# Kernel optimization log

Hardware: AMD Instinct MI355X
Metric: run time of the kernel (lower is better)

The kernel has to match this reference:

```python
import jax, jax.numpy as jnp
import numpy as np

N_NODES = 20000   # N
N_EDGES = 320000  # E (avg degree 16)
T_STEPS = 16      # T
IN_FEATS = 1      # F
HG = 64           # hidden_g
HT = 128          # hidden_t
LN_EPS = 1e-5


def _layer_norm(x, g, b):
    mu = jnp.mean(x, axis=-1, keepdims=True)
    var = jnp.mean((x - mu) ** 2, axis=-1, keepdims=True)
    return (x - mu) * jax.lax.rsqrt(var + LN_EPS) * g + b


def setup_inputs() -> dict:
    key = jax.random.key(0)
    k = jax.random.split(key, 16)
    r = lambda i, shape, s: jax.random.normal(k[i], shape, jnp.float32) * s
    return dict(
        x_seq=jax.random.normal(k[0], (1, T_STEPS, N_NODES, IN_FEATS), jnp.float32),
        edge_index=jax.random.randint(k[1], (2, N_EDGES), 0, N_NODES, dtype=jnp.int32),
        # SAGEConv layer 0: lin_l (aggregated neighbors, has bias) + lin_r (root)
        W_l0=r(2, (IN_FEATS, HG), 0.5), W_r0=r(3, (IN_FEATS, HG), 0.5), b0=jnp.zeros((HG,), jnp.float32),
        ln0_g=jnp.ones((HG,), jnp.float32), ln0_b=jnp.zeros((HG,), jnp.float32),
        # SAGEConv layer 1
        W_l1=r(4, (HG, HG), 0.1), W_r1=r(5, (HG, HG), 0.1), b1=jnp.zeros((HG,), jnp.float32),
        ln1_g=jnp.ones((HG,), jnp.float32), ln1_b=jnp.zeros((HG,), jnp.float32),
        # GRU (torch layout: gates r,z,n stacked along first dim)
        gru_Wih=r(6, (3 * HT, HG), 0.05), gru_Whh=r(7, (3 * HT, HT), 0.05),
        gru_bih=jnp.zeros((3 * HT,), jnp.float32), gru_bhh=jnp.zeros((3 * HT,), jnp.float32),
        # head
        head_W=r(8, (HT, 1), 0.05), head_b=jnp.zeros((1,), jnp.float32),
    )


def reference(x_seq, edge_index, W_l0, W_r0, b0, ln0_g, ln0_b,
              W_l1, W_r1, b1, ln1_g, ln1_b,
              gru_Wih, gru_Whh, gru_bih, gru_bhh, head_W, head_b):
    src, dst = edge_index[0], edge_index[1]
    # in-degree for mean aggregation (clamped to 1, like PyG mean aggr on isolated nodes)
    deg = jnp.clip(jax.ops.segment_sum(jnp.ones((N_EDGES,), jnp.float32), dst,
                                       num_segments=N_NODES), 1.0)[:, None]

    def sage(x, Wl, Wr, b):
        # mean over incoming neighbors, then lin_l(aggr) + lin_r(root)
        agg = jax.ops.segment_sum(x[src], dst, num_segments=N_NODES) / deg
        return agg @ Wl + x @ Wr + b

    def stack(xt):  # xt: (N, F) -> (N, HG); dropout is identity in eval mode
        h = jax.nn.relu(_layer_norm(sage(xt, W_l0, W_r0, b0), ln0_g, ln0_b))
        h = jax.nn.relu(_layer_norm(sage(h, W_l1, W_r1, b1), ln1_g, ln1_b))
        return h

    X = x_seq[0]  # (T, N, F), B == 1
    # scan over timesteps (matches the per-t Python loop, bounds peak memory)
    _, H = jax.lax.scan(lambda c, xt: (c, stack(xt)), None, X)  # H: (T, N, HG)

    def gru_step(h, xt):  # torch GRU cell; batch = N nodes
        gi = xt @ gru_Wih.T + gru_bih
        gh = h @ gru_Whh.T + gru_bhh
        ir, iz, inn = jnp.split(gi, 3, axis=-1)
        hr, hz, hn = jnp.split(gh, 3, axis=-1)
        r = jax.nn.sigmoid(ir + hr)
        z = jax.nn.sigmoid(iz + hz)
        n = jnp.tanh(inn + r * hn)
        return (1.0 - z) * n + z * h, None

    h0 = jnp.zeros((N_NODES, HT), x_seq.dtype)
    hT, _ = jax.lax.scan(gru_step, h0, H)
    y = (hT @ head_W + head_b)[:, 0]  # (N,)
    return y
```

## Files before the change

kernel.cpp:

```cpp
#include <hip/hip_runtime.h>
#include <math.h>

#define NN 20000
#define NE 320000
#define TS 16
#define HG 64
#define HTT 128
#define NG 384
#define LN_EPS 1e-5f
#define ASTR 1032

typedef __attribute__((ext_vector_type(8))) _Float16 f16x8;
typedef __attribute__((ext_vector_type(4))) _Float16 f16x4;
typedef __attribute__((ext_vector_type(4))) float f32x4;

__device__ __forceinline__ float wave_sum64(float v) {
  #pragma unroll
  for (int off = 32; off > 0; off >>= 1) v += __shfl_xor(v, off, 64);
  return v;
}
__device__ __forceinline__ float quad_sum16(float v) {
  #pragma unroll
  for (int off = 1; off < 16; off <<= 1) v += __shfl_xor(v, off, 64);
  return v;
}
__device__ __forceinline__ float fast_sigmoid(float x) {
  return __builtin_amdgcn_rcpf(1.f + __expf(-x));
}
__device__ __forceinline__ float fast_tanh(float x) {
  float e = __expf(-2.f * fabsf(x));
  float th = (1.f - e) * __builtin_amdgcn_rcpf(1.f + e);
  return copysignf(th, x);
}

__global__ __launch_bounds__(256) void k_setup(
    const float* __restrict__ x_seq, float* __restrict__ xT,
    const float* __restrict__ Wih, _Float16* __restrict__ WihF,
    const float* __restrict__ Whh, _Float16* __restrict__ WhhF,
    const float* __restrict__ Wl1, const float* __restrict__ Wr1,
    _Float16* __restrict__ Wchi, _Float16* __restrict__ Wclo,
    const float* __restrict__ Wl0, const float* __restrict__ Wr0,
    const float* __restrict__ b0, const float* __restrict__ g0,
    const float* __restrict__ be0, float* __restrict__ P,
    int* __restrict__ cnt) {
  int gid = blockIdx.x * 256 + threadIdx.x;
  int stride = gridDim.x * 256;
  for (int i = gid; i < NN * TS; i += stride) {
    int t = i / NN, n = i - t * NN;
    xT[n * 16 + t] = x_seq[i];
  }
  for (int i = gid; i < NG * HG; i += stride) WihF[i] = (_Float16)Wih[i];
  for (int i = gid; i < NG * HTT; i += stride) WhhF[i] = (_Float16)Whh[i];
  for (int i = gid; i < HG * 128; i += stride) {
    int n = i >> 7, k = i & 127;
    float x = (k < HG) ? Wl1[k * HG + n] : Wr1[(k - HG) * HG + n];
    _Float16 h = (_Float16)x;
    Wchi[i] = h;
    Wclo[i] = (_Float16)(x - (float)h);
  }
  for (int i = gid; i < NN; i += stride) cnt[i] = 0;
  if (blockIdx.x == 0 && threadIdx.x < 64) {
    int f = threadIdx.x;
    float u = Wl0[f], v = Wr0[f], c = b0[f], g = g0[f];
    float um = wave_sum64(u) * (1.f / 64.f);
    float vm = wave_sum64(v) * (1.f / 64.f);
    float cm = wave_sum64(c) * (1.f / 64.f);
    float uc = u - um, vc = v - vm, cc = c - cm;
    float muu = wave_sum64(uc * uc) * (1.f / 64.f);
    float mvv = wave_sum64(vc * vc) * (1.f / 64.f);
    float mcc = wave_sum64(cc * cc) * (1.f / 64.f);
    float muv = wave_sum64(uc * vc) * (1.f / 64.f);
    float muc = wave_sum64(uc * cc) * (1.f / 64.f);
    float mvc = wave_sum64(vc * cc) * (1.f / 64.f);
    P[f] = uc * g; P[64 + f] = vc * g; P[128 + f] = cc * g; P[192 + f] = be0[f];
    if (f == 0) {
      P[256] = muu; P[257] = mvv; P[258] = mcc;
      P[259] = muv; P[260] = muc; P[261] = mvc;
    }
  }
}

__global__ void k_hist(const int* __restrict__ dst, int* cnt) {
  int e = blockIdx.x * blockDim.x + threadIdx.x;
  if (e < NE) atomicAdd(&cnt[dst[e]], 1);
}

__global__ void k_scan(int* cnt, int* row_ptr, float* deg_inv) {
  __shared__ int s[1024];
  const int PER = 20;
  int tid = threadIdx.x;
  int base = tid * PER;
  int vloc[PER], dloc[PER];
  int sum = 0;
  #pragma unroll
  for (int j = 0; j < PER; j++) {
    int n = base + j;
    int d = (n < NN) ? cnt[n] : 0;
    vloc[j] = sum;
    dloc[j] = d;
    sum += d;
  }
  s[tid] = sum;
  __syncthreads();
  for (int off = 1; off < 1024; off <<= 1) {
    int t = (tid >= off) ? s[tid - off] : 0;
    __syncthreads();
    s[tid] += t;
    __syncthreads();
  }
  int excl = s[tid] - sum;
  #pragma unroll
  for (int j = 0; j < PER; j++) {
    int n = base + j;
    if (n < NN) {
      int rp = excl + vloc[j];
      row_ptr[n] = rp;
      cnt[n] = rp;
      int d = dloc[j];
      deg_inv[n] = 1.0f / (float)((d > 1) ? d : 1);
    }
  }
  if (tid == 1023) row_ptr[NN] = s[1023];
}

__global__ void k_fill(const int* __restrict__ src, const int* __restrict__ dst,
                       int* cursor, int* col) {
  int e = blockIdx.x * blockDim.x + threadIdx.x;
  if (e < NE) {
    int p = atomicAdd(&cursor[dst[e]], 1);
    col[p] = src[e];
  }
}

__global__ __launch_bounds__(256) void k_h0_fused(
    const float* __restrict__ xT,
    const int* __restrict__ row_ptr, const int* __restrict__ col,
    const float* __restrict__ deg_inv,
    const float* __restrict__ P,
    _Float16* __restrict__ h0r,
    _Float16* __restrict__ code) {
  int lane = threadIdx.x & 63;
  int n = blockIdx.x * 4 + (threadIdx.x >> 6);
  int grp = lane >> 4, tl = lane & 15;
  int beg = row_ptr[n];
  int deg = row_ptr[n + 1] - beg;
  float s0 = 0.f, s1 = 0.f;
  int iters = (deg + 7) >> 3;
  for (int it = 0; it < iters; it++) {
    int e0 = it * 8 + grp, e1 = it * 8 + 4 + grp;
    bool v0 = e0 < deg, v1 = e1 < deg;
    int i0 = v0 ? e0 : 0, i1 = v1 ? e1 : 0;
    int c0 = col[beg + i0];
    int c1 = col[beg + i1];
    float x0 = xT[c0 * 16 + tl];
    float x1 = xT[c1 * 16 + tl];
    s0 += v0 ? x0 : 0.f;
    s1 += v1 ? x1 : 0.f;
  }
  float s = s0 + s1;
  s += __shfl_xor(s, 16, 64);
  s += __shfl_xor(s, 32, 64);
  float aggv = s * deg_inv[n];
  float xv = xT[n * 16 + tl];
  float muu = P[256], mvv = P[257], mcc = P[258];
  float muv = P[259], muc = P[260], mvc = P[261];
  if (lane < 16) {
    float a = aggv, x = xv;
    float var = a * a * muu + x * x * mvv + mcc
              + 2.f * (a * x * muv + a * muc + x * mvc);
    float rstd = rsqrtf(var + LN_EPS);
    f16x4 cw;
    cw[0] = (_Float16)(a * rstd);
    cw[1] = (_Float16)(x * rstd);
    cw[2] = (_Float16)rstd;
    cw[3] = (_Float16)0.f;
    *(f16x4*)&code[(size_t)n * 64 + (lane & 7) * 8 + (lane >> 3) * 4] = cw;
  }
  #pragma unroll
  for (int half = 0; half < 2; half++) {
    int c = lane + half * 64;
    int t = c >> 3, f8 = (c & 7) * 8;
    float a = __shfl(aggv, t, 64);
    float x = __shfl(xv, t, 64);
    float var = a * a * muu + x * x * mvv + mcc
              + 2.f * (a * x * muv + a * muc + x * mvc);
    float rstd = rsqrtf(var + LN_EPS);
    f16x8 o;
    #pragma unroll
    for (int j = 0; j < 8; j++) {
      int f = f8 + j;
      float d = a * P[f] + x * P[64 + f] + P[128 + f];
      o[j] = (_Float16)fmaxf(d * rstd + P[192 + f], 0.f);
    }
    *(f16x8*)&h0r[(size_t)n * 1024 + c * 8] = o;
  }
}

__global__ __launch_bounds__(256) void k_sage_fused(
    const _Float16* __restrict__ h0r,
    const int* __restrict__ row_ptr, const int* __restrict__ col,
    const _Float16* __restrict__ code,
    const float* __restrict__ P,
    const _Float16* __restrict__ Wchi, const _Float16* __restrict__ Wclo,
    const float* __restrict__ b1, const float* __restrict__ g1, const float* __restrict__ be1,
    _Float16* __restrict__ Ht_all) {
  __shared__ _Float16 aggL[16 * ASTR];
  int tid = threadIdx.x;
  int lane = tid & 63, wave = tid >> 6;
  int col16 = lane & 15, quad = lane >> 4;
  int m0 = blockIdx.x * 16;

  {
    int f1 = (lane & 7) * 8;
    float Pu[8], Pv[8], Pc[8], Pb[8];
    #pragma unroll
    for (int j = 0; j < 8; j++) {
      Pu[j] = P[f1 + j];
      Pv[j] = P[64 + f1 + j];
      Pc[j] = P[128 + f1 + j];
      Pb[j] = P[192 + f1 + j];
    }
    int codeoff = (lane >> 3) * 8;

    int i4 = lane >> 4;
    int slot = lane & 15;
    int ni = m0 + wave * 4 + i4;
    int beg_i = row_ptr[ni];
    int d_i = row_ptr[ni + 1] - beg_i;
    int cv0 = (slot < d_i) ? col[beg_i + slot] : 0;
    int cv1 = (slot + 16 < d_i) ? col[beg_i + 16 + slot] : 0;
    int dL[4], bgL[4];
    #pragma unroll
    for (int i = 0; i < 4; i++) {
      dL[i] = __builtin_amdgcn_readlane(d_i, i << 4);
      bgL[i] = __builtin_amdgcn_readlane(beg_i, i << 4);
    }

    for (int i = 0; i < 4; i++) {
      float acc1[8], acc2[8];
      #pragma unroll
      for (int j = 0; j < 8; j++) { acc1[j] = 0.f; acc2[j] = 0.f; }

      auto accum = [&](f16x8 cd) {
        float A1 = (float)cd[0], X1 = (float)cd[1], C1 = (float)cd[2];
        float A2 = (float)cd[4], X2 = (float)cd[5], C2 = (float)cd[6];
        #pragma unroll
        for (int j = 0; j < 8; j++) {
          float d1 = fmaf(A1, Pu[j], fmaf(X1, Pv[j], fmaf(C1, Pc[j], Pb[j])));
          acc1[j] += fmaxf(d1, 0.f);
          float d2 = fmaf(A2, Pu[j], fmaf(X2, Pv[j], fmaf(C2, Pc[j], Pb[j])));
          acc2[j] += fmaxf(d2, 0.f);
        }
      };
      auto ldcode = [&](int c) -> f16x8 {
        return *(const f16x8*)(code + (size_t)c * 64 + codeoff);
      };

      int deg = dL[i];
      int m1 = (deg < 16) ? deg : 16;
      int e = 0;
      for (; e + 2 <= m1; e += 2) {
        int c0 = __builtin_amdgcn_readlane(cv0, (i << 4) | e);
        int c1 = __builtin_amdgcn_readlane(cv0, (i << 4) | (e + 1));
        f16x8 cd0 = ldcode(c0);
        f16x8 cd1 = ldcode(c1);
        accum(cd0);
        accum(cd1);
      }
      if (e < m1) {
        int c0 = __builtin_amdgcn_readlane(cv0, (i << 4) | e);
        accum(ldcode(c0));
      }
      if (deg > 16) {
        int m2 = ((deg < 32) ? deg : 32) - 16;
        e = 0;
        for (; e + 2 <= m2; e += 2) {
          int c0 = __builtin_amdgcn_readlane(cv1, (i << 4) | e);
          int c1 = __builtin_amdgcn_readlane(cv1, (i << 4) | (e + 1));
          f16x8 cd0 = ldcode(c0);
          f16x8 cd1 = ldcode(c1);
          accum(cd0);
          accum(cd1);
        }
        if (e < m2) {
          int c0 = __builtin_amdgcn_readlane(cv1, (i << 4) | e);
          accum(ldcode(c0));
        }
        for (int e3 = 32; e3 < deg; e3++)
          accum(ldcode(col[bgL[i] + e3]));
      }

      float di = 1.0f / (float)((deg > 1) ? deg : 1);
      f16x8 o0, o1;
      #pragma unroll
      for (int j = 0; j < 8; j++) {
        o0[j] = (_Float16)(acc1[j] * di);
        o1[j] = (_Float16)(acc2[j] * di);
      }
      int nl = wave * 4 + i;
      *(f16x8*)&aggL[nl * ASTR + lane * 8] = o0;
      *(f16x8*)&aggL[nl * ASTR + 512 + lane * 8] = o1;
    }
  }
  __syncthreads();

  for (int ts = 0; ts < 4; ts++) {
    int t = wave * 4 + ts;
    f32x4 acc[4];
    #pragma unroll
    for (int nt = 0; nt < 4; nt++) acc[nt] = (f32x4){0.f, 0.f, 0.f, 0.f};

    #pragma unroll
    for (int kk = 0; kk < 2; kk++) {
      f16x8 ah = *(const f16x8*)&aggL[col16 * ASTR + t * 64 + kk * 32 + quad * 8];
      #pragma unroll
      for (int nt = 0; nt < 4; nt++) {
        int nf = nt * 16 + col16;
        f16x8 bh = *(const f16x8*)&Wchi[nf * 128 + kk * 32 + quad * 8];
        f16x8 bl = *(const f16x8*)&Wclo[nf * 128 + kk * 32 + quad * 8];
        acc[nt] = __builtin_amdgcn_mfma_f32_16x16x32_f16(ah, bh, acc[nt], 0, 0, 0);
        acc[nt] = __builtin_amdgcn_mfma_f32_16x16x32_f16(ah, bl, acc[nt], 0, 0, 0);
      }
    }
    #pragma unroll
    for (int kk = 0; kk < 2; kk++) {
      f16x8 ah = *(const f16x8*)&h0r[(size_t)(m0 + col16) * 1024 + t * 64 + kk * 32 + quad * 8];
      #pragma unroll
      for (int nt = 0; nt < 4; nt++) {
        int nf = nt * 16 + col16;
        f16x8 bh = *(const f16x8*)&Wchi[nf * 128 + 64 + kk * 32 + quad * 8];
        f16x8 bl = *(const f16x8*)&Wclo[nf * 128 + 64 + kk * 32 + quad * 8];
        acc[nt] = __builtin_amdgcn_mfma_f32_16x16x32_f16(ah, bh, acc[nt], 0, 0, 0);
        acc[nt] = __builtin_amdgcn_mfma_f32_16x16x32_f16(ah, bl, acc[nt], 0, 0, 0);
      }
    }

    float bias[4], gg[4], bb[4];
    #pragma unroll
    for (int nt = 0; nt < 4; nt++) {
      int nf = nt * 16 + col16;
      bias[nt] = b1[nf]; gg[nt] = g1[nf]; bb[nt] = be1[nf];
    }
    #pragma unroll
    for (int r = 0; r < 4; r++) {
      float v[4];
      #pragma unroll
      for (int nt = 0; nt < 4; nt++) v[nt] = acc[nt][r] + bias[nt];
      float s = (v[0] + v[1]) + (v[2] + v[3]);
      float mu = quad_sum16(s) * (1.f / 64.f);
      float sq = 0.f;
      #pragma unroll
      for (int nt = 0; nt < 4; nt++) { v[nt] -= mu; sq += v[nt] * v[nt]; }
      float var = quad_sum16(sq) * (1.f / 64.f);
      float rstd = rsqrtf(var + LN_EPS);
      int m = m0 + quad * 4 + r;
      size_t base = ((size_t)t * NN + m) * HG;
      #pragma unroll
      for (int nt = 0; nt < 4; nt++) {
        float o = fmaxf(v[nt] * rstd * gg[nt] + bb[nt], 0.f);
        Ht_all[base + nt * 16 + col16] = (_Float16)o;
      }
    }
  }
}

__global__ __launch_bounds__(256, 2) void k_gru_all(
    const _Float16* __restrict__ Ht_all,
    const _Float16* __restrict__ WihF,
    const _Float16* __restrict__ WhhF,
    const float* __restrict__ bih, const float* __restrict__ bhh,
    const float* __restrict__ headW, const float* __restrict__ headb,
    float* __restrict__ out) {
  __shared__ _Float16 WihL[NG * 64];
  __shared__ _Float16 hL[2][32 * 128];
  __shared__ float yL[4][32];

  int tid = threadIdx.x;
  int lane = tid & 63, wave = tid >> 6;
  int col16 = lane & 15, quad = lane >> 4;
  int m0 = blockIdx.x * 32;
  int gb = 2 * wave;

  for (int i = tid; i < NG * 8; i += 256) {
    int g = i >> 3, k8 = i & 7;
    *(f16x8*)&WihL[g * 64 + ((k8 + g) & 7) * 8] = *(const f16x8*)&WihF[g * 64 + k8 * 8];
  }
  for (int i = tid; i < 2 * 32 * 128; i += 256) hL[0][i] = (_Float16)0.f;

  int gts[6];
  #pragma unroll
  for (int t6 = 0; t6 < 6; t6++)
    gts[t6] = (t6 < 2) ? (gb + t6) : (t6 < 4) ? (8 + gb + t6 - 2) : (16 + gb + t6 - 4);

  f16x8 wgh[4][6];
  #pragma unroll
  for (int kk = 0; kk < 4; kk++)
    #pragma unroll
    for (int t6 = 0; t6 < 6; t6++)
      wgh[kk][t6] = *(const f16x8*)&WhhF[(size_t)(gts[t6] * 16 + col16) * HTT + kk * 32 + quad * 8];

  int jj[2]; float bR[2], bZ[2], bNi[2], bNh[2], hw[2];
  int waddr[2][4][2];
  #pragma unroll
  for (int js = 0; js < 2; js++) {
    int j = (gb + js) * 16 + col16;
    jj[js] = j;
    bR[js]  = bih[j] + bhh[j];
    bZ[js]  = bih[HTT + j] + bhh[HTT + j];
    bNi[js] = bih[2 * HTT + j];
    bNh[js] = bhh[2 * HTT + j];
    hw[js]  = headW[j];
    #pragma unroll
    for (int mt = 0; mt < 2; mt++)
      #pragma unroll
      for (int r = 0; r < 4; r++) {
        int row = mt * 16 + quad * 4 + r;
        waddr[mt][r][js] = row * 128 + (((j >> 3) + row) & 15) * 8 + (j & 7);
      }
  }
  float hreg[2][4][2];
  #pragma unroll
  for (int mt = 0; mt < 2; mt++)
    #pragma unroll
    for (int r = 0; r < 4; r++) { hreg[mt][r][0] = 0.f; hreg[mt][r][1] = 0.f; }

  size_t aoff[2][2];
  #pragma unroll
  for (int kk = 0; kk < 2; kk++)
    #pragma unroll
    for (int mt = 0; mt < 2; mt++)
      aoff[kk][mt] = (size_t)(m0 + mt * 16 + col16) * HG + kk * 32 + quad * 8;

  __syncthreads();

  for (int t = 0; t < TS; t++) {
    const _Float16* hcur = hL[t & 1];
    _Float16* hnxt = hL[(t + 1) & 1];

    f32x4 acc[8][2];
    #pragma unroll
    for (int a = 0; a < 8; a++) {
      acc[a][0] = (f32x4){0.f, 0.f, 0.f, 0.f};
      acc[a][1] = (f32x4){0.f, 0.f, 0.f, 0.f};
    }

    const _Float16* AH = Ht_all + (size_t)t * NN * HG;
    f16x8 gah[2][2];
    #pragma unroll
    for (int kk = 0; kk < 2; kk++)
      #pragma unroll
      for (int mt = 0; mt < 2; mt++)
        gah[kk][mt] = *(const f16x8*)&AH[aoff[kk][mt]];

    #pragma unroll
    for (int kk = 0; kk < 4; kk++) {
      f16x8 ah[2];
      #pragma unroll
      for (int mt = 0; mt < 2; mt++) {
        int row = mt * 16 + col16;
        int k8 = kk * 4 + quad;
        ah[mt] = *(const f16x8*)&hcur[row * 128 + ((k8 + row) & 15) * 8];
      }
      #pragma unroll
      for (int t6 = 0; t6 < 6; t6++) {
        int ai = (t6 < 4) ? t6 : t6 + 2;
        #pragma unroll
        for (int mt = 0; mt < 2; mt++)
          acc[ai][mt] = __builtin_amdgcn_mfma_f32_16x16x32_f16(ah[mt], wgh[kk][t6], acc[ai][mt], 0, 0, 0);
      }
    }
    #pragma unroll
    for (int kk = 0; kk < 2; kk++) {
      #pragma unroll
      for (int t6 = 0; t6 < 6; t6++) {
        int g = gts[t6] * 16 + col16;
        int k8 = kk * 4 + quad;
        f16x8 b = *(const f16x8*)&WihL[g * 64 + ((k8 + g) & 7) * 8];
        #pragma unroll
        for (int mt = 0; mt < 2; mt++)
          acc[t6][mt] = __builtin_amdgcn_mfma_f32_16x16x32_f16(gah[kk][mt], b, acc[t6][mt], 0, 0, 0);
      }
    }

    #pragma unroll
    for (int mt = 0; mt < 2; mt++) {
      #pragma unroll
      for (int r = 0; r < 4; r++) {
        #pragma unroll
        for (int js = 0; js < 2; js++) {
          float R  = acc[0 + js][mt][r] + bR[js];
          float Z  = acc[2 + js][mt][r] + bZ[js];
          float Ni = acc[4 + js][mt][r] + bNi[js];
          float Nh = acc[6 + js][mt][r] + bNh[js];
          float rg = fast_sigmoid(R);
          float zg = fast_sigmoid(Z);
          float nn = fast_tanh(Ni + rg * Nh);
          float hn = nn + zg * (hreg[mt][r][js] - nn);
          hreg[mt][r][js] = hn;
          hnxt[waddr[mt][r][js]] = (_Float16)hn;
        }
      }
    }
    __syncthreads();
  }

  #pragma unroll
  for (int mt = 0; mt < 2; mt++) {
    #pragma unroll
    for (int r = 0; r < 4; r++) {
      float py = hreg[mt][r][0] * hw[0] + hreg[mt][r][1] * hw[1];
      py = quad_sum16(py);
      if (col16 == 0) yL[wave][mt * 16 + quad * 4 + r] = py;
    }
  }
  __syncthreads();
  if (tid < 32)
    out[m0 + tid] = yL[0][tid] + yL[1][tid] + yL[2][tid] + yL[3][tid] + headb[0];
}

extern "C" void kernel_launch(void* const* d_in, const int* in_sizes, int n_in,
                              void* d_out, int out_size, void* d_ws, size_t ws_size,
                              hipStream_t stream) {
  const float* x_seq = (const float*)d_in[0];
  const int*   edge  = (const int*)d_in[1];
  const float* Wl0   = (const float*)d_in[2];
  const float* Wr0   = (const float*)d_in[3];
  const float* b0    = (const float*)d_in[4];
  const float* g0    = (const float*)d_in[5];
  const float* be0   = (const float*)d_in[6];
  const float* Wl1   = (const float*)d_in[7];
  const float* Wr1   = (const float*)d_in[8];
  const float* b1    = (const float*)d_in[9];
  const float* g1    = (const float*)d_in[10];
  const float* be1   = (const float*)d_in[11];
  const float* Wih   = (const float*)d_in[12];
  const float* Whh   = (const float*)d_in[13];
  const float* bih   = (const float*)d_in[14];
  const float* bhh   = (const float*)d_in[15];
  const float* headW = (const float*)d_in[16];
  const float* headb = (const float*)d_in[17];
  float* out = (float*)d_out;

  const int* srcp = edge;
  const int* dstp = edge + NE;

  char* ws = (char*)d_ws;
  size_t off = 0;
  auto alloc = [&](size_t bytes) -> void* {
    void* p = ws + off;
    off += (bytes + 255) & ~(size_t)255;
    return p;
  };
  int*   cnt     = (int*)alloc(NN * 4);
  int*   row_ptr = (int*)alloc((NN + 1) * 4);
  int*   col     = (int*)alloc(NE * 4);
  float* deg_inv = (float*)alloc(NN * 4);
  float* xT      = (float*)alloc((size_t)NN * TS * 4);
  float* P       = (float*)alloc(512 * 4);
  _Float16* h0r  = (_Float16*)alloc((size_t)NN * 1024 * 2);
  _Float16* code = (_Float16*)alloc((size_t)NN * 64 * 2);
  _Float16* Ht_all = (_Float16*)alloc((size_t)TS * NN * HG * 2);
  _Float16* WihF = (_Float16*)alloc((size_t)NG * HG * 2);
  _Float16* WhhF = (_Float16*)alloc((size_t)NG * HTT * 2);
  _Float16* Wchi = (_Float16*)alloc((size_t)HG * 128 * 2);
  _Float16* Wclo = (_Float16*)alloc((size_t)HG * 128 * 2);
  (void)ws_size; (void)in_sizes; (void)n_in; (void)out_size;

  k_setup<<<1250, 256, 0, stream>>>(x_seq, xT, Wih, WihF, Whh, WhhF,
                                    Wl1, Wr1, Wchi, Wclo,
                                    Wl0, Wr0, b0, g0, be0, P, cnt);
  k_hist<<<(NE + 255) / 256, 256, 0, stream>>>(dstp, cnt);
  k_scan<<<1, 1024, 0, stream>>>(cnt, row_ptr, deg_inv);
  k_fill<<<(NE + 255) / 256, 256, 0, stream>>>(srcp, dstp, cnt, col);
  k_h0_fused<<<NN / 4, 256, 0, stream>>>(xT, row_ptr, col, deg_inv, P, h0r, code);
  k_sage_fused<<<NN / 16, 256, 0, stream>>>(h0r, row_ptr, col, code, P,
                                            Wchi, Wclo, b1, g1, be1, Ht_all);
  k_gru_all<<<NN / 32, 256, 0, stream>>>(Ht_all, WihF, WhhF, bih, bhh,
                                         headW, headb, out);
}
```

Measured before the change: 387.8 us.

## Use packed fp16 math and masked 8-wide neighbor blocks in SAGE aggregation

The neighbor aggregation in the fused SAGE kernel now runs in packed half2 arithmetic (v_pk_fma / pk_max) instead of scalar fp32, which halves the VALU instruction count per neighbor. Neighbors are processed in fixed blocks of 8, with all loads issued ahead and zero masks for padding slots. This replaces the variable-trip loops and increases memory-level parallelism. In exchange, accumulation happens in fp16 with split even/odd accumulators, which costs precision, and low-degree nodes do wasted masked work.

Result: faster. 366.8 us (-5.4%).

```diff
diff --git a/kernel.cpp b/kernel.cpp
--- a/kernel.cpp
+++ b/kernel.cpp
@@ -12,6 +12,7 @@
 
 typedef __attribute__((ext_vector_type(8))) _Float16 f16x8;
 typedef __attribute__((ext_vector_type(4))) _Float16 f16x4;
+typedef __attribute__((ext_vector_type(2))) _Float16 f16x2;
 typedef __attribute__((ext_vector_type(4))) float f32x4;
 
 __device__ __forceinline__ float wave_sum64(float v) {
@@ -211,14 +212,16 @@
   int m0 = blockIdx.x * 16;
 
   {
+    const f16x2 h2z = {(_Float16)0.f, (_Float16)0.f};
+    const f16x2 h2o = {(_Float16)1.f, (_Float16)1.f};
     int f1 = (lane & 7) * 8;
-    float Pu[8], Pv[8], Pc[8], Pb[8];
-    #pragma unroll
-    for (int j = 0; j < 8; j++) {
-      Pu[j] = P[f1 + j];
-      Pv[j] = P[64 + f1 + j];
-      Pc[j] = P[128 + f1 + j];
-      Pb[j] = P[192 + f1 + j];
+    f16x2 Pu2[4], Pv2[4], Pc2[4], Pb2[4];
+    #pragma unroll
+    for (int j = 0; j < 4; j++) {
+      Pu2[j] = (f16x2){(_Float16)P[f1 + 2*j],       (_Float16)P[f1 + 2*j + 1]};
+      Pv2[j] = (f16x2){(_Float16)P[64 + f1 + 2*j],  (_Float16)P[64 + f1 + 2*j + 1]};
+      Pc2[j] = (f16x2){(_Float16)P[128 + f1 + 2*j], (_Float16)P[128 + f1 + 2*j + 1]};
+      Pb2[j] = (f16x2){(_Float16)P[192 + f1 + 2*j], (_Float16)P[192 + f1 + 2*j + 1]};
     }
     int codeoff = (lane >> 3) * 8;
 
@@ -229,78 +232,85 @@
     int d_i = row_ptr[ni + 1] - beg_i;
     int cv0 = (slot < d_i) ? col[beg_i + slot] : 0;
     int cv1 = (slot + 16 < d_i) ? col[beg_i + 16 + slot] : 0;
-    int dL[4], bgL[4];
-    #pragma unroll
+
+    auto ldcode = [&](int c) -> f16x8 {
+      return *(const f16x8*)(code + (size_t)c * 64 + codeoff);
+    };
+
+#define ACCUM(cd, mk, A1, A2)                                              \
+  { f16x2 _A1 = {cd[0], cd[0]}, _X1 = {cd[1], cd[1]}, _C1 = {cd[2], cd[2]};\
+    f16x2 _A2 = {cd[4], cd[4]}, _X2 = {cd[5], cd[5]}, _C2 = {cd[6], cd[6]};\
+    _Pragma("unroll")                                                      \
+    for (int j = 0; j < 4; j++) {                                          \
+      f16x2 d1 = __builtin_elementwise_fma(_A1, Pu2[j],                    \
+                  __builtin_elementwise_fma(_X1, Pv2[j],                   \
+                   __builtin_elementwise_fma(_C1, Pc2[j], Pb2[j])));       \
+      d1 = __builtin_elementwise_max(d1, h2z);                             \
+      A1[j] = __builtin_elementwise_fma(d1, mk, A1[j]);                    \
+      f16x2 d2 = __builtin_elementwise_fma(_A2, Pu2[j],                    \
+                  __builtin_elementwise_fma(_X2, Pv2[j],                   \
+                   __builtin_elementwise_fma(_C2, Pc2[j], Pb2[j])));       \
+      d2 = __builtin_elementwise_max(d2, h2z);                             \
+      A2[j] = __builtin_elementwise_fma(d2, mk, A2[j]);                    \
+    } }
+
+#define BLOCK8(CV, EB, DREL, FULL)                                         \
+  { f16x8 cds[8];                                                          \
+    _Pragma("unroll")                                                      \
+    for (int e = 0; e < 8; e++)                                            \
+      cds[e] = ldcode(__builtin_amdgcn_readlane(CV, ib + (EB) + e));       \
+    _Pragma("unroll")                                                      \
+    for (int e = 0; e < 8; e++) {                                          \
+      f16x2 mk = (FULL) ? h2o : ((((EB) + e) < (DREL)) ? h2o : h2z);       \
+      if (e & 1) ACCUM(cds[e], mk, aO1, aO2)                               \
+      else       ACCUM(cds[e], mk, aE1, aE2)                               \
+    } }
+
     for (int i = 0; i < 4; i++) {
-      dL[i] = __builtin_amdgcn_readlane(d_i, i << 4);
-      bgL[i] = __builtin_amdgcn_readlane(beg_i, i << 4);
-    }
-
-    for (int i = 0; i < 4; i++) {
-      float acc1[8], acc2[8];
-      #pragma unroll
-      for (int j = 0; j < 8; j++) { acc1[j] = 0.f; acc2[j] = 0.f; }
-
-      auto accum = [&](f16x8 cd) {
-        float A1 = (float)cd[0], X1 = (float)cd[1], C1 = (float)cd[2];
-        float A2 = (float)cd[4], X2 = (float)cd[5], C2 = (float)cd[6];
-        #pragma unroll
-        for (int j = 0; j < 8; j++) {
-          float d1 = fmaf(A1, Pu[j], fmaf(X1, Pv[j], fmaf(C1, Pc[j], Pb[j])));
-          acc1[j] += fmaxf(d1, 0.f);
-          float d2 = fmaf(A2, Pu[j], fmaf(X2, Pv[j], fmaf(C2, Pc[j], Pb[j])));
-          acc2[j] += fmaxf(d2, 0.f);
+      int ib = i << 4;
+      int deg = __builtin_amdgcn_readlane(d_i, ib);
+      int bg  = __builtin_amdgcn_readlane(beg_i, ib);
+      f16x2 aE1[4], aO1[4], aE2[4], aO2[4];
+      #pragma unroll
+      for (int j = 0; j < 4; j++) {
+        aE1[j] = h2z; aO1[j] = h2z; aE2[j] = h2z; aO2[j] = h2z;
+      }
+      if (deg >= 16) {
+        BLOCK8(cv0, 0, 16, true)
+        BLOCK8(cv0, 8, 16, true)
+      } else {
+        BLOCK8(cv0, 0, deg, false)
+        BLOCK8(cv0, 8, deg, false)
+      }
+      if (deg > 16) {
+        int dr = deg - 16;
+        if (deg >= 32) {
+          BLOCK8(cv1, 0, 16, true)
+          BLOCK8(cv1, 8, 16, true)
+        } else {
+          BLOCK8(cv1, 0, dr, false)
+          BLOCK8(cv1, 8, dr, false)
         }
-      };
-      auto ldcode = [&](int c) -> f16x8 {
-        return *(const f16x8*)(code + (size_t)c * 64 + codeoff);
-      };
-
-      int deg = dL[i];
-      int m1 = (deg < 16) ? deg : 16;
-      int e = 0;
-      for (; e + 2 <= m1; e += 2) {
-        int c0 = __builtin_amdgcn_readlane(cv0, (i << 4) | e);
-        int c1 = __builtin_amdgcn_readlane(cv0, (i << 4) | (e + 1));
-        f16x8 cd0 = ldcode(c0);
-        f16x8 cd1 = ldcode(c1);
-        accum(cd0);
-        accum(cd1);
-      }
-      if (e < m1) {
-        int c0 = __builtin_amdgcn_readlane(cv0, (i << 4) | e);
-        accum(ldcode(c0));
-      }
-      if (deg > 16) {
-        int m2 = ((deg < 32) ? deg : 32) - 16;
-        e = 0;
-        for (; e + 2 <= m2; e += 2) {
-          int c0 = __builtin_amdgcn_readlane(cv1, (i << 4) | e);
-          int c1 = __builtin_amdgcn_readlane(cv1, (i << 4) | (e + 1));
-          f16x8 cd0 = ldcode(c0);
-          f16x8 cd1 = ldcode(c1);
-          accum(cd0);
-          accum(cd1);
+        for (int e3 = 32; e3 < deg; e3++) {
+          f16x8 cdt = ldcode(col[bg + e3]);
+          ACCUM(cdt, h2o, aE1, aE2)
         }
-        if (e < m2) {
-          int c0 = __builtin_amdgcn_readlane(cv1, (i << 4) | e);
-          accum(ldcode(c0));
-        }
-        for (int e3 = 32; e3 < deg; e3++)
-          accum(ldcode(col[bgL[i] + e3]));
-      }
-
-      float di = 1.0f / (float)((deg > 1) ? deg : 1);
-      f16x8 o0, o1;
-      #pragma unroll
-      for (int j = 0; j < 8; j++) {
-        o0[j] = (_Float16)(acc1[j] * di);
-        o1[j] = (_Float16)(acc2[j] * di);
+      }
+      float dif = 1.0f / (float)((deg > 1) ? deg : 1);
+      _Float16 dih = (_Float16)dif;
+      f16x2 di2 = {dih, dih};
+      union { f16x8 v; f16x2 h[4]; } u0, u1;
+      #pragma unroll
+      for (int j = 0; j < 4; j++) {
+        u0.h[j] = (aE1[j] + aO1[j]) * di2;
+        u1.h[j] = (aE2[j] + aO2[j]) * di2;
       }
       int nl = wave * 4 + i;
-      *(f16x8*)&aggL[nl * ASTR + lane * 8] = o0;
-      *(f16x8*)&aggL[nl * ASTR + 512 + lane * 8] = o1;
-    }
+      *(f16x8*)&aggL[nl * ASTR + lane * 8] = u0.v;
+      *(f16x8*)&aggL[nl * ASTR + 512 + lane * 8] = u1.v;
+    }
+#undef BLOCK8
+#undef ACCUM
   }
   __syncthreads();
 
```
